# Kernel optimization log

Measured on AMD Instinct MI355X. Metric: run time of the kernel, lower is better.

Reference implementation:

```python
import jax, jax.numpy as jnp
import numpy as np

EMBED_DIM = 1024
NUM_HEADS = 16
HEAD_DIM = EMBED_DIM // NUM_HEADS
SCALING = HEAD_DIM ** -0.5
TGT_LEN = 2048
BSZ = 2


def setup_inputs() -> dict:
    key = jax.random.key(0)
    ks = jax.random.split(key, 8)
    E = EMBED_DIM
    query = jax.random.normal(ks[0], (TGT_LEN, BSZ, E), dtype=jnp.float32)
    k_in = jax.random.normal(ks[1], (TGT_LEN, BSZ, E), dtype=jnp.float32)
    v_in = jax.random.normal(ks[2], (TGT_LEN, BSZ, E), dtype=jnp.float32)
    attn_mask = jnp.zeros((TGT_LEN, TGT_LEN), dtype=jnp.float32)
    key_padding_mask = jnp.zeros((1, TGT_LEN, TGT_LEN), dtype=jnp.int32)
    # torch.nn.Linear params: y = x @ W.T + b
    lim_qkv = 1.0 / np.sqrt(E)
    W_qkv = jax.random.uniform(ks[3], (3 * E, E), minval=-lim_qkv, maxval=lim_qkv, dtype=jnp.float32)
    b_qkv = jax.random.uniform(ks[4], (3 * E,), minval=-lim_qkv, maxval=lim_qkv, dtype=jnp.float32)
    W_out = jax.random.uniform(ks[5], (E, E), minval=-lim_qkv, maxval=lim_qkv, dtype=jnp.float32)
    b_out = jax.random.uniform(ks[6], (E,), minval=-lim_qkv, maxval=lim_qkv, dtype=jnp.float32)
    return {"query": query, "key": k_in, "value": v_in, "attn_mask": attn_mask,
            "key_padding_mask": key_padding_mask, "W_qkv": W_qkv, "b_qkv": b_qkv,
            "W_out": W_out, "b_out": b_out}


def reference(query, key, value, attn_mask, key_padding_mask, W_qkv, b_qkv, W_out, b_out):
    # NOTE: original module ignores `key`/`value` args (self-attn from query only).
    T, B, E = query.shape
    H, hd = NUM_HEADS, HEAD_DIM
    neg_inf = jnp.float32(-jnp.inf)
    qkv = query @ W_qkv.T + b_qkv                       # [T, B, 3E]
    qkv = jnp.transpose(qkv.reshape(T, B * H, 3 * hd), (1, 0, 2))  # [BH, T, 3hd]
    q, k, v = jnp.split(qkv, 3, axis=-1)                # each [BH, T, hd]
    aw = jnp.einsum('btd,bsd->bts', q, k) * SCALING     # [BH, T, T]
    # quirk of original: exact-zero scores become -inf
    aw = jnp.where(aw == 0, neg_inf, aw)
    am = jnp.where(attn_mask == 0, jnp.float32(0.0), attn_mask * jnp.float32(-10000.0))
    aw = aw + am
    aw = jnp.where(jnp.swapaxes(key_padding_mask, -2, -1) == 0, aw, neg_inf)
    aw = jax.nn.softmax(aw, axis=-1)
    # dropout p=0.0 -> identity
    out = aw @ v                                        # [BH, T, hd]
    # faithful to original: transpose(0,1) then reshape(bsz, tgt_len, E)
    out = jnp.swapaxes(out, 0, 1).reshape(B, T, E)      # [B, T, E]
    return out @ W_out.T + b_out
```

## Files before the change

kernel.cpp:

```cpp
#include <hip/hip_runtime.h>
#include <math.h>

#define TLEN 2048
#define EMB 1024
#define QKVD 3072
#define NROWS 4096
#define LOG2E 1.4426950408889634f

typedef unsigned short u16;
typedef unsigned int u32;
using frag_ab = __attribute__((ext_vector_type(8))) short;
using f32x4   = __attribute__((ext_vector_type(4))) float;

__device__ __forceinline__ u16 f2bf(float x) {
    u32 u = __builtin_bit_cast(u32, x);
    u = (u + 0x7FFFu + ((u >> 16) & 1u)) >> 16;
    return (u16)u;
}

__device__ __forceinline__ u32 cvt_pk_bf16(float lo, float hi) {
    u32 r;
    asm("v_cvt_pk_bf16_f32 %0, %1, %2" : "=v"(r) : "v"(lo), "v"(hi));
    return r;
}

__device__ __forceinline__ float exp2_hw(float x) {
    float r;
    asm("v_exp_f32 %0, %1" : "=v"(r) : "v"(x));
    return r;
}

#define GLL16(g, l) __builtin_amdgcn_global_load_lds(                         \
    (const __attribute__((address_space(1))) void*)(g),                       \
    (__attribute__((address_space(3))) void*)(l), 16, 0, 0)

__global__ __launch_bounds__(256)
void cvt3_bf16(const float* __restrict__ a, const float* __restrict__ bsrc,
               const float* __restrict__ c, u16* __restrict__ out)
{
    int i = (blockIdx.x * 256 + threadIdx.x) * 8;
    const float* src;
    int off;
    if (i < 4194304)      { src = a;    off = i; }
    else if (i < 7340032) { src = bsrc; off = i - 4194304; }
    else                  { src = c;    off = i - 7340032; }
    float4 x = *reinterpret_cast<const float4*>(src + off);
    float4 y = *reinterpret_cast<const float4*>(src + off + 4);
    union { u16 h[8]; uint4 v; } o;
    o.h[0] = f2bf(x.x); o.h[1] = f2bf(x.y); o.h[2] = f2bf(x.z); o.h[3] = f2bf(x.w);
    o.h[4] = f2bf(y.x); o.h[5] = f2bf(y.y); o.h[6] = f2bf(y.z); o.h[7] = f2bf(y.w);
    *reinterpret_cast<uint4*>(out + i) = o.v;
}

__global__ __launch_bounds__(256)
void build_cmask(const float* __restrict__ am, const int* __restrict__ kpm,
                 float* __restrict__ cm, int* __restrict__ flags)
{
    __shared__ int kt[64][65];
    __shared__ int s_any;
    const int tid = threadIdx.x;
    const int s0 = blockIdx.x * 64, t0 = blockIdx.y * 64;
    if (tid == 0) s_any = 0;
    #pragma unroll
    for (int u = 0; u < 4; ++u) {
        int idx = u * 256 + tid;
        int r  = idx >> 4;
        int cq = (idx & 15) * 4;
        int4 v = *reinterpret_cast<const int4*>(&kpm[(size_t)(s0 + r) * TLEN + t0 + cq]);
        kt[r][cq + 0] = v.x; kt[r][cq + 1] = v.y; kt[r][cq + 2] = v.z; kt[r][cq + 3] = v.w;
    }
    __syncthreads();
    float rbuf[4][4];
    int myany = 0;
    #pragma unroll
    for (int u = 0; u < 4; ++u) {
        int idx = u * 256 + tid;
        int r  = idx >> 4;
        int cq = (idx & 15) * 4;
        float4 a = *reinterpret_cast<const float4*>(&am[(size_t)(t0 + r) * TLEN + s0 + cq]);
        const float av[4] = {a.x, a.y, a.z, a.w};
        #pragma unroll
        for (int c = 0; c < 4; ++c) {
            float t = (av[c] == 0.0f) ? 0.0f : av[c] * -10000.0f;
            if (kt[cq + c][r] != 0) t = -INFINITY;
            rbuf[u][c] = t * LOG2E;
            myany |= (rbuf[u][c] != 0.0f);
        }
    }
    if (myany) s_any = 1;
    __syncthreads();
    if (s_any) {
        #pragma unroll
        for (int u = 0; u < 4; ++u) {
            int idx = u * 256 + tid;
            int r  = idx >> 4;
            int cq = (idx & 15) * 4;
            *reinterpret_cast<float4*>(&cm[(size_t)(t0 + r) * TLEN + s0 + cq]) =
                make_float4(rbuf[u][0], rbuf[u][1], rbuf[u][2], rbuf[u][3]);
        }
    }
    if (tid == 0) flags[blockIdx.y * 32 + blockIdx.x] = s_any;
}

__global__ __launch_bounds__(256)
void transpose_v(const u16* __restrict__ qkv, u16* __restrict__ Vg)
{
    __shared__ u16 tile[64][130];
    const int tid = threadIdx.x;
    const int bh = blockIdx.y;
    const int b = bh >> 4, h = bh & 15;
    const int t0 = blockIdx.x * 128;
    const u16* vsrc = qkv + h * 192 + 128;
    #pragma unroll
    for (int u = 0; u < 4; ++u) {
        int idx = u * 256 + tid;
        int tl = idx >> 3;
        int d0 = (idx & 7) * 8;
        uint4 v = *reinterpret_cast<const uint4*>(
            &vsrc[(size_t)((t0 + tl) * 2 + b) * QKVD + d0]);
        u32 rr[4] = {v.x, v.y, v.z, v.w};
        #pragma unroll
        for (int j = 0; j < 8; ++j)
            tile[d0 + j][tl] = (u16)(rr[j >> 1] >> ((j & 1) * 16));
    }
    __syncthreads();
    #pragma unroll
    for (int u = 0; u < 4; ++u) {
        int idx = u * 256 + tid;
        int d  = idx >> 4;
        int t8 = (idx & 15) * 8;
        union { u16 h[8]; u32 w[4]; uint4 v; } o;
        #pragma unroll
        for (int j = 0; j < 4; ++j)
            o.w[j] = *reinterpret_cast<const u32*>(&tile[d][t8 + 2 * j]);
        *reinterpret_cast<uint4*>(
            &Vg[(size_t)bh * 64 * TLEN + (size_t)d * TLEN + t0 + t8]) = o.v;
    }
}

template <int OUT_BF16, int NF>
__global__ __launch_bounds__(256)
void gemm_nt_mfma(const u16* __restrict__ A, const u16* __restrict__ B,
                  const float* __restrict__ bias, void* __restrict__ Cp,
                  int M, int N, int K)
{
    constexpr int BN = NF * 32;
    __shared__ u16 As[128 * 32];
    __shared__ u16 Bs[BN * 32];
    const int tid  = threadIdx.x;
    const int lane = tid & 63;
    const int w    = tid >> 6;
    const int wr   = w >> 1, wc = w & 1;

    const int nbx = N / BN;
    const int id  = blockIdx.x;
    const int lin = (id & 7) * ((int)gridDim.x >> 3) + (id >> 3);
    const int bm = (lin / nbx) * 128, bn = (lin % nbx) * BN;

    f32x4 acc[4][NF];
    #pragma unroll
    for (int i = 0; i < 4; ++i)
        #pragma unroll
        for (int j = 0; j < NF; ++j)
            acc[i][j] = (f32x4){0.f, 0.f, 0.f, 0.f};

    const int srow = tid >> 2;
    const int skel = (tid & 3) * 8;
    const u16* Ag = A + (size_t)(bm + srow) * K + skel;
    const u16* Bg = B + (size_t)(bn + srow % BN) * K + skel;
    u16* Asl = As + srow * 32 + skel;
    u16* Bsl = Bs + (srow % BN) * 32 + skel;

    const int fr = lane & 15;
    const int fk = (lane >> 4) * 8;

    for (int k0 = 0; k0 < K; k0 += 32) {
        GLL16(Ag + k0, Asl);
        GLL16(Ag + (size_t)64 * K + k0, Asl + 64 * 32);
        GLL16(Bg + k0, Bsl);
        if constexpr (NF == 4) GLL16(Bg + (size_t)64 * K + k0, Bsl + 64 * 32);
        __syncthreads();
        frag_ab af[4], bfr[NF];
        #pragma unroll
        for (int mf = 0; mf < 4; ++mf)
            af[mf] = *reinterpret_cast<const frag_ab*>(&As[(wr * 64 + mf * 16 + fr) * 32 + fk]);
        #pragma unroll
        for (int nf = 0; nf < NF; ++nf)
            bfr[nf] = *reinterpret_cast<const frag_ab*>(
                &Bs[(wc * (NF * 16) + nf * 16 + fr) * 32 + fk]);
        #pragma unroll
        for (int mf = 0; mf < 4; ++mf)
            #pragma unroll
            for (int nf = 0; nf < NF; ++nf)
                acc[mf][nf] = __builtin_amdgcn_mfma_f32_16x16x32_bf16(af[mf], bfr[nf], acc[mf][nf], 0, 0, 0);
        __syncthreads();
    }

    const int col0 = bn + wc * (NF * 16) + fr;
    const int row0 = bm + wr * 64 + (lane >> 4) * 4;
    #pragma unroll
    for (int nf = 0; nf < NF; ++nf) {
        const int col = col0 + nf * 16;
        const float bv = bias[col];
        #pragma unroll
        for (int mf = 0; mf < 4; ++mf) {
            #pragma unroll
            for (int i = 0; i < 4; ++i) {
                const size_t off = (size_t)(row0 + mf * 16 + i) * N + col;
                if (OUT_BF16) ((u16*)Cp)[off]  = f2bf(acc[mf][nf][i] + bv);
                else          ((float*)Cp)[off] = acc[mf][nf][i] + bv;
            }
        }
    }
}

#define ATTN_STEP(CUR, NXT, IT, ITN)                                          \
  {                                                                           \
    GLL16(kbase + (size_t)(((ITN) * 64 + srow) * 2 + b) * QKVD + gsrc,        \
          &Ks[NXT][tid * 8]);                                                 \
    GLL16(kbase + (size_t)(((ITN) * 64 + 32 + srow) * 2 + b) * QKVD + gsrc,   \
          &Ks[NXT][2048 + tid * 8]);                                          \
    GLL16(vgbase + (size_t)srow * TLEN + (ITN) * 64 + gsrc,                   \
          &Vt[NXT][tid * 8]);                                                 \
    GLL16(vgbase + (size_t)(srow + 32) * TLEN + (ITN) * 64 + gsrc,            \
          &Vt[NXT][2048 + tid * 8]);                                          \
    f32x4 sacc[4];                                                            \
    _Pragma("unroll") for (int nf = 0; nf < 4; ++nf)                          \
      sacc[nf] = (f32x4){0.f, 0.f, 0.f, 0.f};                                 \
    __builtin_amdgcn_s_setprio(1);                                            \
    _Pragma("unroll") for (int nf = 0; nf < 4; ++nf) {                        \
      _Pragma("unroll") for (int ks = 0; ks < 2; ++ks) {                      \
        const int krow = nf * 16 + fr;                                        \
        frag_ab bk = *reinterpret_cast<const frag_ab*>(                       \
            &Ks[CUR][krow * 64 + (((4 * ks + fg) ^ (krow & 7)) & 7) * 8]);    \
        sacc[nf] = __builtin_amdgcn_mfma_f32_16x16x32_bf16(bk, aq[ks],        \
                                                           sacc[nf], 0, 0, 0); \
      }                                                                       \
    }                                                                         \
    __builtin_amdgcn_s_setprio(0);                                            \
    float vq[4][4];                                                           \
    _Pragma("unroll") for (int nf = 0; nf < 4; ++nf) {                        \
      _Pragma("unroll") for (int i = 0; i < 4; ++i) {                         \
        const float sv = sacc[nf][i];                                         \
        const float v = fmaf(SSCALE, sv, -24.0f);                             \
        vq[nf][i] = (sv == 0.0f) ? -INFINITY : v;                             \
      }                                                                       \
    }                                                                         \
    if (fmask & (1u << (IT))) {                                               \
      _Pragma("unroll") for (int nf = 0; nf < 4; ++nf) {                      \
        const float4 c4 = *reinterpret_cast<const float4*>(                   \
            &cm2[(size_t)rq * TLEN + (IT) * 64 + nf * 16 + 4 * fg]);          \
        vq[nf][0] += c4.x; vq[nf][1] += c4.y;                                 \
        vq[nf][2] += c4.z; vq[nf][3] += c4.w;                                 \
      }                                                                       \
    }                                                                         \
    float pv[4][4];                                                           \
    _Pragma("unroll") for (int nf = 0; nf < 4; ++nf) {                        \
      _Pragma("unroll") for (int i = 0; i < 4; ++i)                           \
        pv[nf][i] = exp2_hw(vq[nf][i]);                                       \
    }                                                                         \
    u32 pkA[4], pkB[4];                                                       \
    _Pragma("unroll") for (int nf = 0; nf < 4; ++nf) {                        \
      pkA[nf] = cvt_pk_bf16(pv[nf][0], pv[nf][1]);                            \
      pkB[nf] = cvt_pk_bf16(pv[nf][2], pv[nf][3]);                            \
    }                                                                         \
    __builtin_amdgcn_s_setprio(1);                                            \
    _Pragma("unroll") for (int ks = 0; ks < 2; ++ks) {                        \
      u32 d0 = pkA[2 * ks], d1 = pkB[2 * ks];                                 \
      u32 s0 = pkA[2 * ks + 1], s1 = pkB[2 * ks + 1];                         \
      asm("v_permlane32_swap_b32 %0, %1" : "+v"(d0), "+v"(s0));               \
      asm("v_permlane32_swap_b32 %0, %1" : "+v"(d1), "+v"(s1));               \
      const u32 sel0 = odd ? d0 : s0;                                         \
      const u32 sel1 = odd ? d1 : s1;                                         \
      const u32 r0_ = __builtin_amdgcn_ds_swizzle(sel0, 0x401F);              \
      const u32 r1_ = __builtin_amdgcn_ds_swizzle(sel1, 0x401F);              \
      union { u32 wq[4]; frag_ab f; } pau;                                    \
      pau.wq[0] = odd ? r0_ : d0;                                             \
      pau.wq[1] = odd ? r1_ : d1;                                             \
      pau.wq[2] = odd ? s0 : r0_;                                             \
      pau.wq[3] = odd ? s1 : r1_;                                             \
      _Pragma("unroll") for (int nf = 0; nf < 4; ++nf) {                      \
        const int drow = nf * 16 + fr;                                        \
        frag_ab bv = *reinterpret_cast<const frag_ab*>(                       \
            &Vt[CUR][drow * 64 + (((4 * ks + fg) ^ (drow & 7)) & 7) * 8]);    \
        oacc[nf] = __builtin_amdgcn_mfma_f32_16x16x32_bf16(pau.f, bv,         \
                                                           oacc[nf], 0, 0, 0); \
      }                                                                       \
      osum = __builtin_amdgcn_mfma_f32_16x16x32_bf16(pau.f, fones, osum,      \
                                                     0, 0, 0);                \
    }                                                                         \
    __builtin_amdgcn_s_setprio(0);                                            \
    asm volatile("s_waitcnt vmcnt(0)" ::: "memory");                          \
    __builtin_amdgcn_s_barrier();                                             \
  }

__global__ __launch_bounds__(256, 4)
void attn_mfma(const u16* __restrict__ qkv, const float* __restrict__ cm2,
               const int* __restrict__ flags, const u16* __restrict__ Vg,
               u16* __restrict__ X2)
{
    __shared__ u16 QP[64 * 64];
    __shared__ u16 Ks[2][64 * 64];
    __shared__ u16 Vt[2][64 * 64];

    const int tid  = threadIdx.x;
    const int lane = tid & 63;
    const int w    = tid >> 6;

    const int id  = blockIdx.x;
    const int lin = (id & 7) * 128 + (id >> 3);
    const int bh  = lin >> 5;
    const int tt  = lin & 31;
    const int b = bh >> 4, h = bh & 15;
    const int t0 = tt * 64;

    const u16* qbase  = qkv + h * 192;
    const u16* kbase  = qkv + h * 192 + 64;
    const u16* vgbase = Vg + (size_t)bh * 64 * TLEN;

    const int srow = tid >> 3;
    const int sgl  = tid & 7;
    const int gsrc = ((sgl ^ (srow & 7)) & 7) * 8;
    const int fr = lane & 15;
    const int fg = lane >> 4;
    const bool odd = (lane & 16) != 0;
    const int rq = t0 + w * 16 + fr;

    frag_ab fones;
    #pragma unroll
    for (int j = 0; j < 8; ++j) fones[j] = (short)0x3F80;

    const int* fl = flags + tt * 32;
    int fv = 0;
    if (lane < 32) fv = fl[lane];
    const u32 fmask = (u32)__ballot(fv != 0);

    GLL16(qbase + (size_t)((t0 + srow) * 2 + b) * QKVD + gsrc, &QP[tid * 8]);
    GLL16(qbase + (size_t)((t0 + 32 + srow) * 2 + b) * QKVD + gsrc, &QP[2048 + tid * 8]);
    GLL16(kbase + (size_t)(srow * 2 + b) * QKVD + gsrc, &Ks[0][tid * 8]);
    GLL16(kbase + (size_t)((32 + srow) * 2 + b) * QKVD + gsrc, &Ks[0][2048 + tid * 8]);
    GLL16(vgbase + (size_t)srow * TLEN + gsrc, &Vt[0][tid * 8]);
    GLL16(vgbase + (size_t)(srow + 32) * TLEN + gsrc, &Vt[0][2048 + tid * 8]);
    __syncthreads();

    frag_ab aq[2];
    #pragma unroll
    for (int ks = 0; ks < 2; ++ks) {
        const int row = w * 16 + fr;
        aq[ks] = *reinterpret_cast<const frag_ab*>(
            &QP[row * 64 + (((4 * ks + fg) ^ (row & 7)) & 7) * 8]);
    }

    f32x4 oacc[4];
    #pragma unroll
    for (int nf = 0; nf < 4; ++nf) oacc[nf] = (f32x4){0.f, 0.f, 0.f, 0.f};
    f32x4 osum = (f32x4){0.f, 0.f, 0.f, 0.f};

    const float SSCALE = 0.125f * LOG2E;

    for (int it = 0; it < 32; it += 2) {
        const int it1 = it + 1;
        ATTN_STEP(0, 1, it, it1)
        ATTN_STEP(1, 0, it1, (it1 < 31 ? it1 + 1 : 31))
    }

    #pragma unroll
    for (int i = 0; i < 4; ++i) {
        const int t = t0 + w * 16 + fg * 4 + i;
        const int rout = ((t >= 1024) ? 2048 : 0) + 2 * (t & 1023) + b;
        const float inv = 1.f / osum[i];
        #pragma unroll
        for (int nf = 0; nf < 4; ++nf)
            X2[(size_t)rout * EMB + h * 64 + nf * 16 + fr] = f2bf(oacc[nf][i] * inv);
    }
}

extern "C" void kernel_launch(void* const* d_in, const int* in_sizes, int n_in,
                              void* d_out, int out_size, void* d_ws, size_t ws_size,
                              hipStream_t stream)
{
    const float* query = (const float*)d_in[0];
    const float* am    = (const float*)d_in[3];
    const int*   kpm   = (const int*)d_in[4];
    const float* Wqkv  = (const float*)d_in[5];
    const float* bqkv  = (const float*)d_in[6];
    const float* Wout  = (const float*)d_in[7];
    const float* bout  = (const float*)d_in[8];
    float* out = (float*)d_out;

    char* ws = (char*)d_ws;
    u16*   qkv_bf  = (u16*)(ws);
    u16*   x2_bf   = (u16*)(ws + 25165824);
    float* cmask   = (float*)(ws + 33554432);
    u16*   q_bf    = (u16*)(ws + 50331648);
    u16*   wqkv_bf = (u16*)(ws + 58720256);
    u16*   wout_bf = (u16*)(ws + 65011712);
    int*   flags   = (int*)(ws + 67108864);
    u16*   v_tr    = (u16*)(ws + 67112960);

    cvt3_bf16<<<4096, 256, 0, stream>>>(query, Wqkv, Wout, q_bf);
    build_cmask<<<dim3(32, 32), 256, 0, stream>>>(am, kpm, cmask, flags);

    gemm_nt_mfma<1, 4><<<768, 256, 0, stream>>>(q_bf, wqkv_bf, bqkv, qkv_bf,
                                                NROWS, QKVD, EMB);
    transpose_v<<<dim3(16, 32), 256, 0, stream>>>(qkv_bf, v_tr);
    attn_mfma<<<1024, 256, 0, stream>>>(qkv_bf, cmask, flags, v_tr, x2_bf);
    gemm_nt_mfma<0, 2><<<512, 256, 0, stream>>>(x2_bf, wout_bf, bout, out,
                                                NROWS, EMB, EMB);
}
```

Before: 150.9 us.

## Fuse V transpose into QKV GEMM epilogue and merge prep kernels

The bf16 conversion and mask-building kernels are merged into a single prep launch. The V transpose kernel is removed: the QKV GEMM epilogue now writes V columns straight into the transposed [bh, d, t] layout and writes only the Q/K columns to the qkv buffer. The attention kernel moves to one flat shared-memory buffer with precomputed swizzle offsets. This saves two launches and a full read and write of V, at the cost of strided 2-byte scatter stores in the GEMM epilogue.

```diff
diff --git a/kernel.cpp b/kernel.cpp
--- a/kernel.cpp
+++ b/kernel.cpp
@@ -35,31 +35,32 @@
     (__attribute__((address_space(3))) void*)(l), 16, 0, 0)
 
 __global__ __launch_bounds__(256)
-void cvt3_bf16(const float* __restrict__ a, const float* __restrict__ bsrc,
-               const float* __restrict__ c, u16* __restrict__ out)
-{
-    int i = (blockIdx.x * 256 + threadIdx.x) * 8;
-    const float* src;
-    int off;
-    if (i < 4194304)      { src = a;    off = i; }
-    else if (i < 7340032) { src = bsrc; off = i - 4194304; }
-    else                  { src = c;    off = i - 7340032; }
-    float4 x = *reinterpret_cast<const float4*>(src + off);
-    float4 y = *reinterpret_cast<const float4*>(src + off + 4);
-    union { u16 h[8]; uint4 v; } o;
-    o.h[0] = f2bf(x.x); o.h[1] = f2bf(x.y); o.h[2] = f2bf(x.z); o.h[3] = f2bf(x.w);
-    o.h[4] = f2bf(y.x); o.h[5] = f2bf(y.y); o.h[6] = f2bf(y.z); o.h[7] = f2bf(y.w);
-    *reinterpret_cast<uint4*>(out + i) = o.v;
-}
-
-__global__ __launch_bounds__(256)
-void build_cmask(const float* __restrict__ am, const int* __restrict__ kpm,
-                 float* __restrict__ cm, int* __restrict__ flags)
+void prep(const float* __restrict__ qa, const float* __restrict__ wqkv,
+          const float* __restrict__ wout, u16* __restrict__ out,
+          const float* __restrict__ am, const int* __restrict__ kpm,
+          float* __restrict__ cm, int* __restrict__ flags)
 {
     __shared__ int kt[64][65];
     __shared__ int s_any;
     const int tid = threadIdx.x;
-    const int s0 = blockIdx.x * 64, t0 = blockIdx.y * 64;
+    const int bid = blockIdx.x;
+    if (bid < 4096) {
+        int i = (bid * 256 + tid) * 8;
+        const float* src;
+        int off;
+        if (i < 4194304)      { src = qa;   off = i; }
+        else if (i < 7340032) { src = wqkv; off = i - 4194304; }
+        else                  { src = wout; off = i - 7340032; }
+        float4 x = *reinterpret_cast<const float4*>(src + off);
+        float4 y = *reinterpret_cast<const float4*>(src + off + 4);
+        union { u16 h[8]; uint4 v; } o;
+        o.h[0] = f2bf(x.x); o.h[1] = f2bf(x.y); o.h[2] = f2bf(x.z); o.h[3] = f2bf(x.w);
+        o.h[4] = f2bf(y.x); o.h[5] = f2bf(y.y); o.h[6] = f2bf(y.z); o.h[7] = f2bf(y.w);
+        *reinterpret_cast<uint4*>(out + i) = o.v;
+        return;
+    }
+    const int id2 = bid - 4096;
+    const int s0 = (id2 & 31) * 64, t0 = (id2 >> 5) * 64;
     if (tid == 0) s_any = 0;
     #pragma unroll
     for (int u = 0; u < 4; ++u) {
@@ -99,50 +100,14 @@
                 make_float4(rbuf[u][0], rbuf[u][1], rbuf[u][2], rbuf[u][3]);
         }
     }
-    if (tid == 0) flags[blockIdx.y * 32 + blockIdx.x] = s_any;
-}
-
-__global__ __launch_bounds__(256)
-void transpose_v(const u16* __restrict__ qkv, u16* __restrict__ Vg)
-{
-    __shared__ u16 tile[64][130];
-    const int tid = threadIdx.x;
-    const int bh = blockIdx.y;
-    const int b = bh >> 4, h = bh & 15;
-    const int t0 = blockIdx.x * 128;
-    const u16* vsrc = qkv + h * 192 + 128;
-    #pragma unroll
-    for (int u = 0; u < 4; ++u) {
-        int idx = u * 256 + tid;
-        int tl = idx >> 3;
-        int d0 = (idx & 7) * 8;
-        uint4 v = *reinterpret_cast<const uint4*>(
-            &vsrc[(size_t)((t0 + tl) * 2 + b) * QKVD + d0]);
-        u32 rr[4] = {v.x, v.y, v.z, v.w};
-        #pragma unroll
-        for (int j = 0; j < 8; ++j)
-            tile[d0 + j][tl] = (u16)(rr[j >> 1] >> ((j & 1) * 16));
-    }
-    __syncthreads();
-    #pragma unroll
-    for (int u = 0; u < 4; ++u) {
-        int idx = u * 256 + tid;
-        int d  = idx >> 4;
-        int t8 = (idx & 15) * 8;
-        union { u16 h[8]; u32 w[4]; uint4 v; } o;
-        #pragma unroll
-        for (int j = 0; j < 4; ++j)
-            o.w[j] = *reinterpret_cast<const u32*>(&tile[d][t8 + 2 * j]);
-        *reinterpret_cast<uint4*>(
-            &Vg[(size_t)bh * 64 * TLEN + (size_t)d * TLEN + t0 + t8]) = o.v;
-    }
-}
-
-template <int OUT_BF16, int NF>
+    if (tid == 0) flags[id2] = s_any;
+}
+
+template <int OUT_MODE, int NF>
 __global__ __launch_bounds__(256)
 void gemm_nt_mfma(const u16* __restrict__ A, const u16* __restrict__ B,
                   const float* __restrict__ bias, void* __restrict__ Cp,
-                  int M, int N, int K)
+                  u16* __restrict__ Vg, int M, int N, int K)
 {
     constexpr int BN = NF * 32;
     __shared__ u16 As[128 * 32];
@@ -202,37 +167,59 @@
     for (int nf = 0; nf < NF; ++nf) {
         const int col = col0 + nf * 16;
         const float bv = bias[col];
-        #pragma unroll
-        for (int mf = 0; mf < 4; ++mf) {
+        if constexpr (OUT_MODE == 0) {
             #pragma unroll
-            for (int i = 0; i < 4; ++i) {
-                const size_t off = (size_t)(row0 + mf * 16 + i) * N + col;
-                if (OUT_BF16) ((u16*)Cp)[off]  = f2bf(acc[mf][nf][i] + bv);
-                else          ((float*)Cp)[off] = acc[mf][nf][i] + bv;
+            for (int mf = 0; mf < 4; ++mf)
+                #pragma unroll
+                for (int i = 0; i < 4; ++i)
+                    ((float*)Cp)[(size_t)(row0 + mf * 16 + i) * N + col] = acc[mf][nf][i] + bv;
+        } else {
+            const u32 q6 = (u32)col >> 6;
+            const u32 h = (q6 * 0xAAABu) >> 17;
+            const int seg = col - (int)h * 192;
+            if (seg < 128) {
+                #pragma unroll
+                for (int mf = 0; mf < 4; ++mf)
+                    #pragma unroll
+                    for (int i = 0; i < 4; ++i)
+                        ((u16*)Cp)[(size_t)(row0 + mf * 16 + i) * N + col] =
+                            f2bf(acc[mf][nf][i] + bv);
+            } else {
+                const int d = seg - 128;
+                #pragma unroll
+                for (int mf = 0; mf < 4; ++mf)
+                    #pragma unroll
+                    for (int i = 0; i < 4; ++i) {
+                        const int row = row0 + mf * 16 + i;
+                        Vg[(size_t)(((row & 1) * 16 + (int)h) * 64 + d) * TLEN + (row >> 1)] =
+                            f2bf(acc[mf][nf][i] + bv);
+                    }
             }
         }
     }
 }
+
+#define SM_KS 8192
+#define SM_VT 24576
 
 #define ATTN_STEP(CUR, NXT, IT, ITN)                                          \
   {                                                                           \
     GLL16(kbase + (size_t)(((ITN) * 64 + srow) * 2 + b) * QKVD + gsrc,        \
-          &Ks[NXT][tid * 8]);                                                 \
+          smem + SM_KS + (NXT) * 8192 + tid * 16);                            \
     GLL16(kbase + (size_t)(((ITN) * 64 + 32 + srow) * 2 + b) * QKVD + gsrc,   \
-          &Ks[NXT][2048 + tid * 8]);                                          \
+          smem + SM_KS + (NXT) * 8192 + 4096 + tid * 16);                     \
     GLL16(vgbase + (size_t)srow * TLEN + (ITN) * 64 + gsrc,                   \
-          &Vt[NXT][tid * 8]);                                                 \
+          smem + SM_VT + (NXT) * 8192 + tid * 16);                            \
     GLL16(vgbase + (size_t)(srow + 32) * TLEN + (ITN) * 64 + gsrc,            \
-          &Vt[NXT][2048 + tid * 8]);                                          \
+          smem + SM_VT + (NXT) * 8192 + 4096 + tid * 16);                     \
     f32x4 sacc[4];                                                            \
     _Pragma("unroll") for (int nf = 0; nf < 4; ++nf)                          \
       sacc[nf] = (f32x4){0.f, 0.f, 0.f, 0.f};                                 \
     __builtin_amdgcn_s_setprio(1);                                            \
     _Pragma("unroll") for (int nf = 0; nf < 4; ++nf) {                        \
       _Pragma("unroll") for (int ks = 0; ks < 2; ++ks) {                      \
-        const int krow = nf * 16 + fr;                                        \
         frag_ab bk = *reinterpret_cast<const frag_ab*>(                       \
-            &Ks[CUR][krow * 64 + (((4 * ks + fg) ^ (krow & 7)) & 7) * 8]);    \
+            smem + SM_KS + (CUR) * 8192 + nf * 2048 + (ks ? kb1 : kb0));      \
         sacc[nf] = __builtin_amdgcn_mfma_f32_16x16x32_bf16(bk, aq[ks],        \
                                                            sacc[nf], 0, 0, 0); \
       }                                                                       \
@@ -280,9 +267,8 @@
       pau.wq[2] = odd ? s0 : r0_;                                             \
       pau.wq[3] = odd ? s1 : r1_;                                             \
       _Pragma("unroll") for (int nf = 0; nf < 4; ++nf) {                      \
-        const int drow = nf * 16 + fr;                                        \
         frag_ab bv = *reinterpret_cast<const frag_ab*>(                       \
-            &Vt[CUR][drow * 64 + (((4 * ks + fg) ^ (drow & 7)) & 7) * 8]);    \
+            smem + SM_VT + (CUR) * 8192 + nf * 2048 + (ks ? kb1 : kb0));      \
         oacc[nf] = __builtin_amdgcn_mfma_f32_16x16x32_bf16(pau.f, bv,         \
                                                            oacc[nf], 0, 0, 0); \
       }                                                                       \
@@ -299,9 +285,7 @@
                const int* __restrict__ flags, const u16* __restrict__ Vg,
                u16* __restrict__ X2)
 {
-    __shared__ u16 QP[64 * 64];
-    __shared__ u16 Ks[2][64 * 64];
-    __shared__ u16 Vt[2][64 * 64];
+    __shared__ __attribute__((aligned(16))) char smem[40960];
 
     const int tid  = threadIdx.x;
     const int lane = tid & 63;
@@ -326,6 +310,9 @@
     const bool odd = (lane & 16) != 0;
     const int rq = t0 + w * 16 + fr;
 
+    const int kb0 = fr * 128 + (((fg) ^ (fr & 7)) & 7) * 16;
+    const int kb1 = fr * 128 + (((4 + fg) ^ (fr & 7)) & 7) * 16;
+
     frag_ab fones;
     #pragma unroll
     for (int j = 0; j < 8; ++j) fones[j] = (short)0x3F80;
@@ -335,21 +322,17 @@
     if (lane < 32) fv = fl[lane];
     const u32 fmask = (u32)__ballot(fv != 0);
 
-    GLL16(qbase + (size_t)((t0 + srow) * 2 + b) * QKVD + gsrc, &QP[tid * 8]);
-    GLL16(qbase + (size_t)((t0 + 32 + srow) * 2 + b) * QKVD + gsrc, &QP[2048 + tid * 8]);
-    GLL16(kbase + (size_t)(srow * 2 + b) * QKVD + gsrc, &Ks[0][tid * 8]);
-    GLL16(kbase + (size_t)((32 + srow) * 2 + b) * QKVD + gsrc, &Ks[0][2048 + tid * 8]);
-    GLL16(vgbase + (size_t)srow * TLEN + gsrc, &Vt[0][tid * 8]);
-    GLL16(vgbase + (size_t)(srow + 32) * TLEN + gsrc, &Vt[0][2048 + tid * 8]);
+    GLL16(qbase + (size_t)((t0 + srow) * 2 + b) * QKVD + gsrc, smem + tid * 16);
+    GLL16(qbase + (size_t)((t0 + 32 + srow) * 2 + b) * QKVD + gsrc, smem + 4096 + tid * 16);
+    GLL16(kbase + (size_t)(srow * 2 + b) * QKVD + gsrc, smem + SM_KS + tid * 16);
+    GLL16(kbase + (size_t)((32 + srow) * 2 + b) * QKVD + gsrc, smem + SM_KS + 4096 + tid * 16);
+    GLL16(vgbase + (size_t)srow * TLEN + gsrc, smem + SM_VT + tid * 16);
+    GLL16(vgbase + (size_t)(srow + 32) * TLEN + gsrc, smem + SM_VT + 4096 + tid * 16);
     __syncthreads();
 
     frag_ab aq[2];
-    #pragma unroll
-    for (int ks = 0; ks < 2; ++ks) {
-        const int row = w * 16 + fr;
-        aq[ks] = *reinterpret_cast<const frag_ab*>(
-            &QP[row * 64 + (((4 * ks + fg) ^ (row & 7)) & 7) * 8]);
-    }
+    aq[0] = *reinterpret_cast<const frag_ab*>(smem + w * 2048 + kb0);
+    aq[1] = *reinterpret_cast<const frag_ab*>(smem + w * 2048 + kb1);
 
     f32x4 oacc[4];
     #pragma unroll
@@ -398,13 +381,11 @@
     int*   flags   = (int*)(ws + 67108864);
     u16*   v_tr    = (u16*)(ws + 67112960);
 
-    cvt3_bf16<<<4096, 256, 0, stream>>>(query, Wqkv, Wout, q_bf);
-    build_cmask<<<dim3(32, 32), 256, 0, stream>>>(am, kpm, cmask, flags);
-
-    gemm_nt_mfma<1, 4><<<768, 256, 0, stream>>>(q_bf, wqkv_bf, bqkv, qkv_bf,
-                                                NROWS, QKVD, EMB);
-    transpose_v<<<dim3(16, 32), 256, 0, stream>>>(qkv_bf, v_tr);
+    prep<<<5120, 256, 0, stream>>>(query, Wqkv, Wout, q_bf, am, kpm, cmask, flags);
+
+    gemm_nt_mfma<2, 4><<<768, 256, 0, stream>>>(q_bf, wqkv_bf, bqkv, qkv_bf,
+                                                v_tr, NROWS, QKVD, EMB);
     attn_mfma<<<1024, 256, 0, stream>>>(qkv_bf, cmask, flags, v_tr, x2_bf);
     gemm_nt_mfma<0, 2><<<512, 256, 0, stream>>>(x2_bf, wout_bf, bout, out,
-                                                NROWS, EMB, EMB);
-}
+                                                nullptr, NROWS, EMB, EMB);
+}
```

Result: faster. 133.9 us (-11.3%).
